# Performance work log

Hardware: AMD Instinct MI355X
Metric: run time of the kernel (lower is better)

The kernel has to match this reference:

```python
import jax, jax.numpy as jnp
import numpy as np

T, H, I, E, K = 4096, 2048, 1408, 8, 2  # tokens, hidden, intermediate, experts, top_k


def setup_inputs() -> dict:
    key = jax.random.key(0)
    ks = jax.random.split(key, 6)
    hidden_states = jax.random.normal(ks[0], (T, H), dtype=jnp.float32)
    gate_weight = jax.random.normal(ks[1], (E, H), dtype=jnp.float32) * 0.02  # fp32 gate, per source assert
    w13_weight = jax.random.randint(ks[2], (E, 2 * I, H), -127, 128, dtype=jnp.int8)
    w13_weight_scale = jax.random.uniform(ks[3], (E, 2 * I), dtype=jnp.float32, minval=0.5, maxval=1.5) * 0.005
    w2_weight = jax.random.randint(ks[4], (E, H, I), -127, 128, dtype=jnp.int8)
    w2_weight_scale = jax.random.uniform(ks[5], (E, H), dtype=jnp.float32, minval=0.5, maxval=1.5) * 0.005
    return dict(hidden_states=hidden_states, gate_weight=gate_weight,
                w13_weight=w13_weight, w13_weight_scale=w13_weight_scale,
                w2_weight=w2_weight, w2_weight_scale=w2_weight_scale)


def _dynamic_quant_i8(x):
    # per-token dynamic symmetric int8: scale = max|x|/127 (smooth scales default to ones)
    s = jnp.maximum(jnp.max(jnp.abs(x), axis=-1, keepdims=True) / 127.0, 1e-8)
    q = jnp.clip(jnp.round(x / s), -127.0, 127.0)
    return q, s


def reference(hidden_states, gate_weight, w13_weight, w13_weight_scale, w2_weight, w2_weight_scale):
    # --- gating: fp32 linear + topk softmax (renormalize=True) ---
    logits = hidden_states @ gate_weight.T              # [T, E]
    probs = jax.nn.softmax(logits, axis=-1)
    topv, topi = jax.lax.top_k(probs, K)                # [T, K]
    gates = topv / jnp.sum(topv, axis=-1, keepdims=True)
    # dense routing weights [T, E]: gate value where expert selected, else 0
    route = jnp.zeros((T, E), hidden_states.dtype).at[jnp.arange(T)[:, None], topi].add(gates)

    # --- dynamic per-token int8 quant of routed input (same token value for each of its K copies) ---
    q_in, s_in = _dynamic_quant_i8(hidden_states)       # [T, H], [T, 1]

    # --- grouped w8a8 GEMM (fc1) -> SwiGLU -> requant -> grouped GEMM (fc2) -> weighted combine ---
    def step(acc, xs):
        w13, s13, w2, s2w, r = xs                       # per-expert weights / route column [T]
        h1 = (q_in @ w13.T.astype(jnp.float32)) * s_in * s13[None, :]   # dequant fc1: [T, 2I]
        g, u = h1[:, :I], h1[:, I:]
        act = jax.nn.silu(g) * u                        # SwiGLU
        q_a, s_a = _dynamic_quant_i8(act)
        h2 = (q_a @ w2.T.astype(jnp.float32)) * s_a * s2w[None, :]      # dequant fc2: [T, H]
        return acc + r[:, None] * h2, None

    acc0 = jnp.zeros_like(hidden_states)
    out, _ = jax.lax.scan(step, acc0,
                          (w13_weight, w13_weight_scale, w2_weight, w2_weight_scale, route.T))
    return out
```

## Files before the change

### kernel.cpp

```cpp
#include <hip/hip_runtime.h>

#define T_TOK 4096
#define H_DIM 2048
#define I_DIM 1408
#define E_NUM 8
#define NI2   (2 * I_DIM)

typedef int v4i __attribute__((ext_vector_type(4)));

#define GLD_LDS16(gptr, lptr)                                                        \
  __builtin_amdgcn_global_load_lds(                                                  \
      (const __attribute__((address_space(1))) void*)(gptr),                         \
      (__attribute__((address_space(3))) void*)(lptr), 16, 0, 0)

__global__ __launch_bounds__(256) void pack_all(const int* __restrict__ w13,
                                                const int* __restrict__ w2,
                                                signed char* __restrict__ qw13,
                                                signed char* __restrict__ qw2,
                                                int n16a, int n16tot) {
  int i = blockIdx.x * 256 + threadIdx.x;
  if (i >= n16tot) return;
  const int* src;
  signed char* dst;
  int j;
  if (i < n16a) { src = w13; dst = qw13; j = i; }
  else          { src = w2;  dst = qw2;  j = i - n16a; }
  const int4* s4 = (const int4*)src + (size_t)j * 4;
  int4 v0 = s4[0], v1 = s4[1], v2 = s4[2], v3 = s4[3];
  union { signed char c[16]; int4 v; } pk;
  pk.c[0] = (signed char)v0.x;  pk.c[1] = (signed char)v0.y;
  pk.c[2] = (signed char)v0.z;  pk.c[3] = (signed char)v0.w;
  pk.c[4] = (signed char)v1.x;  pk.c[5] = (signed char)v1.y;
  pk.c[6] = (signed char)v1.z;  pk.c[7] = (signed char)v1.w;
  pk.c[8] = (signed char)v2.x;  pk.c[9] = (signed char)v2.y;
  pk.c[10] = (signed char)v2.z; pk.c[11] = (signed char)v2.w;
  pk.c[12] = (signed char)v3.x; pk.c[13] = (signed char)v3.y;
  pk.c[14] = (signed char)v3.z; pk.c[15] = (signed char)v3.w;
  ((int4*)dst)[j] = pk.v;
}

__global__ __launch_bounds__(256) void gate_route_quant(
    const float* __restrict__ hs, const float* __restrict__ gw,
    signed char* __restrict__ qin, float* __restrict__ s_in,
    int* __restrict__ tope, float* __restrict__ gts) {
  const int t = blockIdx.x;
  const int tid = threadIdx.x;
  const int lane = tid & 63;
  const int wave = tid >> 6;
  const float* row = hs + (size_t)t * H_DIM;

  const float4* r4 = (const float4*)row + tid * 2;
  float4 xa = r4[0], xb = r4[1];
  float x[8] = {xa.x, xa.y, xa.z, xa.w, xb.x, xb.y, xb.z, xb.w};

  double pd[8];
  for (int e = 0; e < 8; e++) pd[e] = 0.0;
  float am = 0.f;
  for (int j = 0; j < 8; j++) {
    float v = x[j];
    am = fmaxf(am, fabsf(v));
    int col = tid * 8 + j;
    for (int e = 0; e < 8; e++)
      pd[e] += (double)v * (double)gw[e * H_DIM + col];
  }
  for (int e = 0; e < 8; e++)
    for (int s = 32; s; s >>= 1) pd[e] += __shfl_down(pd[e], s);
  for (int s = 32; s; s >>= 1) am = fmaxf(am, __shfl_down(am, s));

  __shared__ double sred[4][8];
  __shared__ float sam[4];
  __shared__ float sbc;
  if (lane == 0) {
    for (int e = 0; e < 8; e++) sred[wave][e] = pd[e];
    sam[wave] = am;
  }
  __syncthreads();
  if (tid == 0) {
    float l[8];
    for (int e = 0; e < 8; e++)
      l[e] = (float)(sred[0][e] + sred[1][e] + sred[2][e] + sred[3][e]);
    float amx = fmaxf(fmaxf(sam[0], sam[1]), fmaxf(sam[2], sam[3]));
    float s = fmaxf(amx / 127.0f, 1e-8f);
    s_in[t] = s;
    sbc = s;
    int i1 = 0;
    for (int e = 1; e < 8; e++) if (l[e] > l[i1]) i1 = e;
    int i2 = -1;
    for (int e = 0; e < 8; e++) {
      if (e == i1) continue;
      if (i2 < 0 || l[e] > l[i2]) i2 = e;
    }
    float d = expf(l[i2] - l[i1]);
    tope[2 * t] = i1;     gts[2 * t] = 1.0f / (1.0f + d);
    tope[2 * t + 1] = i2; gts[2 * t + 1] = d / (1.0f + d);
  }
  __syncthreads();
  float s = sbc;
  union { signed char c[8]; unsigned long long u; } pk;
  for (int j = 0; j < 8; j++) {
    float q = rintf(x[j] / s);
    q = fminf(127.f, fmaxf(-127.f, q));
    pk.c[j] = (signed char)q;
  }
  ((unsigned long long*)(qin + (size_t)t * H_DIM))[tid] = pk.u;
}

__global__ __launch_bounds__(256) void build_lists(
    const int* __restrict__ tope, int* __restrict__ tok_list,
    int* __restrict__ epos, int* __restrict__ cnt) {
  const int e = blockIdx.x;
  const int tid = threadIdx.x;
  const int lane = tid & 63;
  const int wave = tid >> 6;
  __shared__ int wsum[4];
  __shared__ int base_s;
  if (tid == 0) base_s = 0;
  __syncthreads();
  for (int t0 = 0; t0 < T_TOK; t0 += 256) {
    int t = t0 + tid;
    int i1 = tope[2 * t], i2 = tope[2 * t + 1];
    int slot = (i1 == e) ? 0 : ((i2 == e) ? 1 : -1);
    unsigned long long m = __ballot(slot >= 0);
    int wpre = __popcll(m & ((1ull << lane) - 1ull));
    if (lane == 0) wsum[wave] = __popcll(m);
    __syncthreads();
    int pre = wpre;
    for (int w = 0; w < wave; w++) pre += wsum[w];
    int total = wsum[0] + wsum[1] + wsum[2] + wsum[3];
    int b = base_s;
    if (slot >= 0) {
      int pos = b + pre;
      tok_list[e * T_TOK + pos] = t;
      epos[2 * t + slot] = (e << 16) | pos;
    }
    __syncthreads();
    if (tid == 0) base_s = b + total;
  }
  __syncthreads();
  if (tid == 0) cnt[e] = base_s;
}

__global__ void calc_off(const int* __restrict__ cnt, int* __restrict__ off) {
  if (threadIdx.x == 0) {
    int s = 0;
    for (int e = 0; e < E_NUM; e++) { off[e] = s; s += cnt[e]; }
  }
}

__global__ __launch_bounds__(256, 3) void gemm1_silu(
    const signed char* __restrict__ qw13, const signed char* __restrict__ qin,
    const float* __restrict__ s_in, const float* __restrict__ s13,
    const int* __restrict__ tok_list, const int* __restrict__ cnt,
    const int* __restrict__ off, float* __restrict__ act,
    unsigned int* __restrict__ amax) {
  const int e = blockIdx.z;
  const int ce = cnt[e];
  const int m0 = blockIdx.y * 64;
  if (m0 >= ce) return;
  const int n0 = blockIdx.x * 128;

  __shared__ __align__(16) signed char As[64 * 64];
  __shared__ __align__(16) signed char Bg[128 * 64];
  __shared__ __align__(16) signed char Bu[128 * 64];

  const int tid = threadIdx.x;
  const int lane = tid & 63;
  const int wave = tid >> 6;
  const int quad = lane >> 4;
  const int ln = lane & 15;

  const int* tl = tok_list + e * T_TOK;
  const int rowA = tid >> 2;
  const int kc = (tid & 3) * 16;

  const int tA = tl[min(m0 + rowA, ce - 1)];
  const signed char* gA = qin + (size_t)tA * H_DIM + kc;
  const signed char* w13e = qw13 + (size_t)e * NI2 * H_DIM;
  const signed char* gBg0 = w13e + (size_t)(n0 + rowA) * H_DIM + kc;
  const signed char* gBg1 = w13e + (size_t)(n0 + rowA + 64) * H_DIM + kc;
  const signed char* gBu0 = gBg0 + (size_t)I_DIM * H_DIM;
  const signed char* gBu1 = gBg1 + (size_t)I_DIM * H_DIM;
  const int ldsA = tid * 16;
  const int lds1 = 4096 + ldsA;

  v4i accg[4][2], accu[4][2];
  v4i zero = {0, 0, 0, 0};
#pragma unroll
  for (int i = 0; i < 4; i++)
#pragma unroll
    for (int j = 0; j < 2; j++) { accg[i][j] = zero; accu[i][j] = zero; }

  for (int k0 = 0; k0 < H_DIM; k0 += 64) {
    __syncthreads();
    GLD_LDS16(gA + k0, As + ldsA);
    GLD_LDS16(gBg0 + k0, Bg + ldsA);
    GLD_LDS16(gBg1 + k0, Bg + lds1);
    GLD_LDS16(gBu0 + k0, Bu + ldsA);
    GLD_LDS16(gBu1 + k0, Bu + lds1);
    __syncthreads();

    v4i af[4], bgf[2], buf_[2];
#pragma unroll
    for (int mt = 0; mt < 4; mt++)
      af[mt] = *(const v4i*)(As + (mt * 16 + ln) * 64 + quad * 16);
#pragma unroll
    for (int nt = 0; nt < 2; nt++) {
      bgf[nt] = *(const v4i*)(Bg + (wave * 32 + nt * 16 + ln) * 64 + quad * 16);
      buf_[nt] = *(const v4i*)(Bu + (wave * 32 + nt * 16 + ln) * 64 + quad * 16);
    }
#pragma unroll
    for (int mt = 0; mt < 4; mt++)
#pragma unroll
      for (int nt = 0; nt < 2; nt++) {
        accg[mt][nt] = __builtin_amdgcn_mfma_i32_16x16x64_i8(af[mt], bgf[nt], accg[mt][nt], 0, 0, 0);
        accu[mt][nt] = __builtin_amdgcn_mfma_i32_16x16x64_i8(af[mt], buf_[nt], accu[mt][nt], 0, 0, 0);
      }
  }

  const float* s13e = s13 + e * NI2;
  float sg[2], su[2];
  int ncol[2];
#pragma unroll
  for (int nt = 0; nt < 2; nt++) {
    int n = n0 + wave * 32 + nt * 16 + ln;
    ncol[nt] = n;
    sg[nt] = s13e[n];
    su[nt] = s13e[I_DIM + n];
  }
  const int offe = off[e];
#pragma unroll
  for (int mt = 0; mt < 4; mt++) {
#pragma unroll
    for (int r = 0; r < 4; r++) {
      int mrel = m0 + mt * 16 + quad * 4 + r;
      bool valid = mrel < ce;
      int tok = tl[valid ? mrel : 0];
      float si = s_in[tok];
      int crow = offe + mrel;
      float* arow = act + (size_t)crow * I_DIM;
      float am = 0.f;
#pragma unroll
      for (int nt = 0; nt < 2; nt++) {
        float g = (float)accg[mt][nt][r] * si * sg[nt];
        float u = (float)accu[mt][nt][r] * si * su[nt];
        float a = g / (1.0f + expf(-g)) * u;
        if (valid) arow[ncol[nt]] = a;
        am = fmaxf(am, fabsf(a));
      }
      for (int s = 1; s < 16; s <<= 1) am = fmaxf(am, __shfl_xor(am, s, 16));
      if (valid && ln == 0) atomicMax(amax + crow, __float_as_uint(am));
    }
  }
}

__global__ __launch_bounds__(256) void quant_act(const float* __restrict__ act,
                                                 const unsigned int* __restrict__ amax,
                                                 signed char* __restrict__ qa,
                                                 float* __restrict__ s_a) {
  const int r = blockIdx.x;
  float am = __uint_as_float(amax[r]);
  float s = fmaxf(am / 127.0f, 1e-8f);
  if (threadIdx.x == 0) s_a[r] = s;
  const float* arow = act + (size_t)r * I_DIM;
  signed char* qrow = qa + (size_t)r * I_DIM;
  for (int j = threadIdx.x; j < I_DIM; j += 256) {
    float q = rintf(arow[j] / s);
    q = fminf(127.f, fmaxf(-127.f, q));
    qrow[j] = (signed char)q;
  }
}

__global__ __launch_bounds__(256, 4) void gemm2_h2(
    const signed char* __restrict__ qw2, const signed char* __restrict__ qa,
    const float* __restrict__ s_a, const float* __restrict__ s2w,
    const int* __restrict__ cnt, const int* __restrict__ off,
    float* __restrict__ h2s) {
  const int e = blockIdx.z;
  const int ce = cnt[e];
  const int m0 = blockIdx.y * 64;
  if (m0 >= ce) return;
  const int n0 = blockIdx.x * 128;
  const int offe = off[e];

  __shared__ __align__(16) signed char As[64 * 64];
  __shared__ __align__(16) signed char Bs[128 * 64];

  const int tid = threadIdx.x;
  const int lane = tid & 63;
  const int wave = tid >> 6;
  const int quad = lane >> 4;
  const int ln = lane & 15;

  const int rowA = tid >> 2;
  const int kc = (tid & 3) * 16;

  const signed char* gA = qa + (size_t)(offe + min(m0 + rowA, ce - 1)) * I_DIM + kc;
  const signed char* w2e = qw2 + (size_t)e * H_DIM * I_DIM;
  const signed char* gB0 = w2e + (size_t)(n0 + rowA) * I_DIM + kc;
  const signed char* gB1 = w2e + (size_t)(n0 + rowA + 64) * I_DIM + kc;
  const int ldsA = tid * 16;
  const int lds1 = 4096 + ldsA;

  v4i acc[4][2];
  v4i zero = {0, 0, 0, 0};
#pragma unroll
  for (int i = 0; i < 4; i++)
#pragma unroll
    for (int j = 0; j < 2; j++) acc[i][j] = zero;

  for (int k0 = 0; k0 < I_DIM; k0 += 64) {
    __syncthreads();
    GLD_LDS16(gA + k0, As + ldsA);
    GLD_LDS16(gB0 + k0, Bs + ldsA);
    GLD_LDS16(gB1 + k0, Bs + lds1);
    __syncthreads();

    v4i af[4], bf[2];
#pragma unroll
    for (int mt = 0; mt < 4; mt++)
      af[mt] = *(const v4i*)(As + (mt * 16 + ln) * 64 + quad * 16);
#pragma unroll
    for (int nt = 0; nt < 2; nt++)
      bf[nt] = *(const v4i*)(Bs + (wave * 32 + nt * 16 + ln) * 64 + quad * 16);
#pragma unroll
    for (int mt = 0; mt < 4; mt++)
#pragma unroll
      for (int nt = 0; nt < 2; nt++)
        acc[mt][nt] = __builtin_amdgcn_mfma_i32_16x16x64_i8(af[mt], bf[nt], acc[mt][nt], 0, 0, 0);
  }

  const float* s2e = s2w + e * H_DIM;
  float sw[2];
  int ncol[2];
#pragma unroll
  for (int nt = 0; nt < 2; nt++) {
    int n = n0 + wave * 32 + nt * 16 + ln;
    ncol[nt] = n;
    sw[nt] = s2e[n];
  }
#pragma unroll
  for (int mt = 0; mt < 4; mt++) {
#pragma unroll
    for (int r = 0; r < 4; r++) {
      int mrel = m0 + mt * 16 + quad * 4 + r;
      if (mrel >= ce) continue;
      float sa = s_a[offe + mrel];
      float* orow = h2s + (size_t)(offe + mrel) * H_DIM;
#pragma unroll
      for (int nt = 0; nt < 2; nt++)
        orow[ncol[nt]] = (float)acc[mt][nt][r] * sa * sw[nt];
    }
  }
}

__global__ __launch_bounds__(256) void gather_out(
    const float* __restrict__ h2s, const int* __restrict__ epos,
    const float* __restrict__ gts, const int* __restrict__ off,
    float* __restrict__ out) {
  const int t = blockIdx.x;
  int a = epos[2 * t], b = epos[2 * t + 1];
  float g1 = gts[2 * t], g2 = gts[2 * t + 1];
  int r1 = off[a >> 16] + (a & 0xffff);
  int r2 = off[b >> 16] + (b & 0xffff);
  const float4* R1 = (const float4*)(h2s + (size_t)r1 * H_DIM);
  const float4* R2 = (const float4*)(h2s + (size_t)r2 * H_DIM);
  float4* O = (float4*)(out + (size_t)t * H_DIM);
  for (int c = threadIdx.x; c < H_DIM / 4; c += 256) {
    float4 x = R1[c], y = R2[c];
    float4 z;
    z.x = g1 * x.x + g2 * y.x;
    z.y = g1 * x.y + g2 * y.y;
    z.z = g1 * x.z + g2 * y.z;
    z.w = g1 * x.w + g2 * y.w;
    O[c] = z;
  }
}

extern "C" void kernel_launch(void* const* d_in, const int* in_sizes, int n_in,
                              void* d_out, int out_size, void* d_ws, size_t ws_size,
                              hipStream_t stream) {
  const float* hs = (const float*)d_in[0];
  const float* gw = (const float*)d_in[1];
  const int* w13 = (const int*)d_in[2];
  const float* s13 = (const float*)d_in[3];
  const int* w2 = (const int*)d_in[4];
  const float* s2w = (const float*)d_in[5];
  float* out = (float*)d_out;

  char* ws = (char*)d_ws;
  size_t o = 0;
  auto take = [&](size_t b) {
    char* p = ws + o;
    o += (b + 255) & ~(size_t)255;
    return p;
  };
  signed char* qw13 = (signed char*)take((size_t)E_NUM * NI2 * H_DIM);
  signed char* qin = (signed char*)take((size_t)T_TOK * H_DIM);
  float* act = (float*)take((size_t)T_TOK * 2 * I_DIM * 4);
  float* h2s = (float*)qw13;
  signed char* qw2 = (signed char*)take((size_t)E_NUM * H_DIM * I_DIM);
  signed char* qa = (signed char*)take((size_t)T_TOK * 2 * I_DIM);
  float* sin_ = (float*)take((size_t)T_TOK * 4);
  float* sa = (float*)take((size_t)T_TOK * 2 * 4);
  unsigned int* amax = (unsigned int*)take((size_t)T_TOK * 2 * 4);
  int* tokl = (int*)take((size_t)E_NUM * T_TOK * 4);
  int* tope = (int*)take((size_t)T_TOK * 2 * 4);
  int* epos = (int*)take((size_t)T_TOK * 2 * 4);
  float* gts = (float*)take((size_t)T_TOK * 2 * 4);
  int* cnt = (int*)take(E_NUM * 4);
  int* off = (int*)take(E_NUM * 4);

  hipMemsetAsync(amax, 0, (size_t)T_TOK * 2 * 4, stream);

  {
    int n16a = E_NUM * NI2 * H_DIM / 16;
    int n16b = E_NUM * H_DIM * I_DIM / 16;
    int n16tot = n16a + n16b;
    pack_all<<<(n16tot + 255) / 256, 256, 0, stream>>>(w13, w2, qw13, qw2, n16a, n16tot);
  }
  gate_route_quant<<<T_TOK, 256, 0, stream>>>(hs, gw, qin, sin_, tope, gts);
  build_lists<<<E_NUM, 256, 0, stream>>>(tope, tokl, epos, cnt);
  calc_off<<<1, 64, 0, stream>>>(cnt, off);
  {
    dim3 g(I_DIM / 128, T_TOK / 64, E_NUM);
    gemm1_silu<<<g, 256, 0, stream>>>(qw13, qin, sin_, s13, tokl, cnt, off, act, amax);
  }
  quant_act<<<T_TOK * 2, 256, 0, stream>>>(act, amax, qa, sa);
  {
    dim3 g(H_DIM / 128, T_TOK / 64, E_NUM);
    gemm2_h2<<<g, 256, 0, stream>>>(qw2, qa, sa, s2w, cnt, off, h2s);
  }
  gather_out<<<T_TOK, 256, 0, stream>>>(h2s, epos, gts, off, out);
}
```

Before: 584.1 us.

## Replace LDS staging with direct register loads and double-buffered MFMA loops

Both grouped GEMMs drop the shared-memory tiles and __syncthreads barriers. Each wave now loads its A and B MFMA fragments straight from global memory into registers, using a two-stage register double buffer so loads for the next k-chunk overlap the current MFMAs. The grid is also reordered so blockIdx.x walks the token (M) tiles, which may keep the same weight columns hot in cache across neighbouring blocks. In exchange, the A tile is no longer shared across the four waves, so each wave refetches it from global memory or cache, and register pressure rises.

```diff
diff --git a/kernel.cpp b/kernel.cpp
--- a/kernel.cpp
+++ b/kernel.cpp
@@ -7,11 +7,6 @@
 #define NI2   (2 * I_DIM)
 
 typedef int v4i __attribute__((ext_vector_type(4)));
-
-#define GLD_LDS16(gptr, lptr)                                                        \
-  __builtin_amdgcn_global_load_lds(                                                  \
-      (const __attribute__((address_space(1))) void*)(gptr),                         \
-      (__attribute__((address_space(3))) void*)(lptr), 16, 0, 0)
 
 __global__ __launch_bounds__(256) void pack_all(const int* __restrict__ w13,
                                                 const int* __restrict__ w2,
@@ -155,33 +150,30 @@
     unsigned int* __restrict__ amax) {
   const int e = blockIdx.z;
   const int ce = cnt[e];
-  const int m0 = blockIdx.y * 64;
+  const int m0 = blockIdx.x * 64;
   if (m0 >= ce) return;
-  const int n0 = blockIdx.x * 128;
-
-  __shared__ __align__(16) signed char As[64 * 64];
-  __shared__ __align__(16) signed char Bg[128 * 64];
-  __shared__ __align__(16) signed char Bu[128 * 64];
-
-  const int tid = threadIdx.x;
-  const int lane = tid & 63;
-  const int wave = tid >> 6;
+  const int wave = threadIdx.x >> 6;
+  const int lane = threadIdx.x & 63;
   const int quad = lane >> 4;
   const int ln = lane & 15;
+  const int n0 = blockIdx.y * 128 + wave * 32;
 
   const int* tl = tok_list + e * T_TOK;
-  const int rowA = tid >> 2;
-  const int kc = (tid & 3) * 16;
-
-  const int tA = tl[min(m0 + rowA, ce - 1)];
-  const signed char* gA = qin + (size_t)tA * H_DIM + kc;
   const signed char* w13e = qw13 + (size_t)e * NI2 * H_DIM;
-  const signed char* gBg0 = w13e + (size_t)(n0 + rowA) * H_DIM + kc;
-  const signed char* gBg1 = w13e + (size_t)(n0 + rowA + 64) * H_DIM + kc;
-  const signed char* gBu0 = gBg0 + (size_t)I_DIM * H_DIM;
-  const signed char* gBu1 = gBg1 + (size_t)I_DIM * H_DIM;
-  const int ldsA = tid * 16;
-  const int lds1 = 4096 + ldsA;
+
+  const signed char* ap[4];
+#pragma unroll
+  for (int mt = 0; mt < 4; mt++) {
+    int mrel = min(m0 + mt * 16 + ln, ce - 1);
+    ap[mt] = qin + (size_t)tl[mrel] * H_DIM + quad * 16;
+  }
+  const signed char* bgp[2];
+  const signed char* bup[2];
+#pragma unroll
+  for (int nt = 0; nt < 2; nt++) {
+    bgp[nt] = w13e + (size_t)(n0 + nt * 16 + ln) * H_DIM + quad * 16;
+    bup[nt] = bgp[nt] + (size_t)I_DIM * H_DIM;
+  }
 
   v4i accg[4][2], accu[4][2];
   v4i zero = {0, 0, 0, 0};
@@ -190,39 +182,45 @@
 #pragma unroll
     for (int j = 0; j < 2; j++) { accg[i][j] = zero; accu[i][j] = zero; }
 
-  for (int k0 = 0; k0 < H_DIM; k0 += 64) {
-    __syncthreads();
-    GLD_LDS16(gA + k0, As + ldsA);
-    GLD_LDS16(gBg0 + k0, Bg + ldsA);
-    GLD_LDS16(gBg1 + k0, Bg + lds1);
-    GLD_LDS16(gBu0 + k0, Bu + ldsA);
-    GLD_LDS16(gBu1 + k0, Bu + lds1);
-    __syncthreads();
-
-    v4i af[4], bgf[2], buf_[2];
-#pragma unroll
-    for (int mt = 0; mt < 4; mt++)
-      af[mt] = *(const v4i*)(As + (mt * 16 + ln) * 64 + quad * 16);
-#pragma unroll
-    for (int nt = 0; nt < 2; nt++) {
-      bgf[nt] = *(const v4i*)(Bg + (wave * 32 + nt * 16 + ln) * 64 + quad * 16);
-      buf_[nt] = *(const v4i*)(Bu + (wave * 32 + nt * 16 + ln) * 64 + quad * 16);
-    }
-#pragma unroll
-    for (int mt = 0; mt < 4; mt++)
-#pragma unroll
-      for (int nt = 0; nt < 2; nt++) {
-        accg[mt][nt] = __builtin_amdgcn_mfma_i32_16x16x64_i8(af[mt], bgf[nt], accg[mt][nt], 0, 0, 0);
-        accu[mt][nt] = __builtin_amdgcn_mfma_i32_16x16x64_i8(af[mt], buf_[nt], accu[mt][nt], 0, 0, 0);
-      }
-  }
+  v4i aA[4], gA[2], uA[2];
+  v4i aB[4], gB[2], uB[2];
+
+#define LOADSET(Ar, Gr, Ur, K)                                         \
+  {                                                                    \
+    _Pragma("unroll") for (int mt = 0; mt < 4; mt++)                   \
+        Ar[mt] = *(const v4i*)(ap[mt] + (K));                          \
+    _Pragma("unroll") for (int nt = 0; nt < 2; nt++) {                 \
+      Gr[nt] = *(const v4i*)(bgp[nt] + (K));                           \
+      Ur[nt] = *(const v4i*)(bup[nt] + (K));                           \
+    }                                                                  \
+  }
+#define MFMASET(Ar, Gr, Ur)                                            \
+  {                                                                    \
+    _Pragma("unroll") for (int mt = 0; mt < 4; mt++)                   \
+        _Pragma("unroll") for (int nt = 0; nt < 2; nt++) {             \
+      accg[mt][nt] = __builtin_amdgcn_mfma_i32_16x16x64_i8(            \
+          Ar[mt], Gr[nt], accg[mt][nt], 0, 0, 0);                      \
+      accu[mt][nt] = __builtin_amdgcn_mfma_i32_16x16x64_i8(            \
+          Ar[mt], Ur[nt], accu[mt][nt], 0, 0, 0);                      \
+    }                                                                  \
+  }
+
+  LOADSET(aA, gA, uA, 0)
+  for (int k0 = 0; k0 < H_DIM; k0 += 128) {
+    LOADSET(aB, gB, uB, k0 + 64)
+    MFMASET(aA, gA, uA)
+    if (k0 + 128 < H_DIM) LOADSET(aA, gA, uA, k0 + 128)
+    MFMASET(aB, gB, uB)
+  }
+#undef LOADSET
+#undef MFMASET
 
   const float* s13e = s13 + e * NI2;
   float sg[2], su[2];
   int ncol[2];
 #pragma unroll
   for (int nt = 0; nt < 2; nt++) {
-    int n = n0 + wave * 32 + nt * 16 + ln;
+    int n = n0 + nt * 16 + ln;
     ncol[nt] = n;
     sg[nt] = s13e[n];
     su[nt] = s13e[I_DIM + n];
@@ -277,29 +275,27 @@
     float* __restrict__ h2s) {
   const int e = blockIdx.z;
   const int ce = cnt[e];
-  const int m0 = blockIdx.y * 64;
+  const int m0 = blockIdx.x * 64;
   if (m0 >= ce) return;
-  const int n0 = blockIdx.x * 128;
   const int offe = off[e];
-
-  __shared__ __align__(16) signed char As[64 * 64];
-  __shared__ __align__(16) signed char Bs[128 * 64];
-
-  const int tid = threadIdx.x;
-  const int lane = tid & 63;
-  const int wave = tid >> 6;
+  const int wave = threadIdx.x >> 6;
+  const int lane = threadIdx.x & 63;
   const int quad = lane >> 4;
   const int ln = lane & 15;
-
-  const int rowA = tid >> 2;
-  const int kc = (tid & 3) * 16;
-
-  const signed char* gA = qa + (size_t)(offe + min(m0 + rowA, ce - 1)) * I_DIM + kc;
+  const int n0 = blockIdx.y * 128 + wave * 32;
+
   const signed char* w2e = qw2 + (size_t)e * H_DIM * I_DIM;
-  const signed char* gB0 = w2e + (size_t)(n0 + rowA) * I_DIM + kc;
-  const signed char* gB1 = w2e + (size_t)(n0 + rowA + 64) * I_DIM + kc;
-  const int ldsA = tid * 16;
-  const int lds1 = 4096 + ldsA;
+
+  const signed char* ap[4];
+#pragma unroll
+  for (int mt = 0; mt < 4; mt++) {
+    int mrel = min(m0 + mt * 16 + ln, ce - 1);
+    ap[mt] = qa + (size_t)(offe + mrel) * I_DIM + quad * 16;
+  }
+  const signed char* bp[2];
+#pragma unroll
+  for (int nt = 0; nt < 2; nt++)
+    bp[nt] = w2e + (size_t)(n0 + nt * 16 + ln) * I_DIM + quad * 16;
 
   v4i acc[4][2];
   v4i zero = {0, 0, 0, 0};
@@ -308,33 +304,39 @@
 #pragma unroll
     for (int j = 0; j < 2; j++) acc[i][j] = zero;
 
-  for (int k0 = 0; k0 < I_DIM; k0 += 64) {
-    __syncthreads();
-    GLD_LDS16(gA + k0, As + ldsA);
-    GLD_LDS16(gB0 + k0, Bs + ldsA);
-    GLD_LDS16(gB1 + k0, Bs + lds1);
-    __syncthreads();
-
-    v4i af[4], bf[2];
-#pragma unroll
-    for (int mt = 0; mt < 4; mt++)
-      af[mt] = *(const v4i*)(As + (mt * 16 + ln) * 64 + quad * 16);
-#pragma unroll
-    for (int nt = 0; nt < 2; nt++)
-      bf[nt] = *(const v4i*)(Bs + (wave * 32 + nt * 16 + ln) * 64 + quad * 16);
-#pragma unroll
-    for (int mt = 0; mt < 4; mt++)
-#pragma unroll
-      for (int nt = 0; nt < 2; nt++)
-        acc[mt][nt] = __builtin_amdgcn_mfma_i32_16x16x64_i8(af[mt], bf[nt], acc[mt][nt], 0, 0, 0);
-  }
+  v4i aA[4], bA[2], aB[4], bB[2];
+
+#define LOADSET2(Ar, Br, K)                                            \
+  {                                                                    \
+    _Pragma("unroll") for (int mt = 0; mt < 4; mt++)                   \
+        Ar[mt] = *(const v4i*)(ap[mt] + (K));                          \
+    _Pragma("unroll") for (int nt = 0; nt < 2; nt++)                   \
+        Br[nt] = *(const v4i*)(bp[nt] + (K));                          \
+  }
+#define MFMASET2(Ar, Br)                                               \
+  {                                                                    \
+    _Pragma("unroll") for (int mt = 0; mt < 4; mt++)                   \
+        _Pragma("unroll") for (int nt = 0; nt < 2; nt++)               \
+            acc[mt][nt] = __builtin_amdgcn_mfma_i32_16x16x64_i8(       \
+                Ar[mt], Br[nt], acc[mt][nt], 0, 0, 0);                 \
+  }
+
+  LOADSET2(aA, bA, 0)
+  for (int k0 = 0; k0 < I_DIM; k0 += 128) {
+    LOADSET2(aB, bB, k0 + 64)
+    MFMASET2(aA, bA)
+    if (k0 + 128 < I_DIM) LOADSET2(aA, bA, k0 + 128)
+    MFMASET2(aB, bB)
+  }
+#undef LOADSET2
+#undef MFMASET2
 
   const float* s2e = s2w + e * H_DIM;
   float sw[2];
   int ncol[2];
 #pragma unroll
   for (int nt = 0; nt < 2; nt++) {
-    int n = n0 + wave * 32 + nt * 16 + ln;
+    int n = n0 + nt * 16 + ln;
     ncol[nt] = n;
     sw[nt] = s2e[n];
   }
@@ -422,12 +424,12 @@
   build_lists<<<E_NUM, 256, 0, stream>>>(tope, tokl, epos, cnt);
   calc_off<<<1, 64, 0, stream>>>(cnt, off);
   {
-    dim3 g(I_DIM / 128, T_TOK / 64, E_NUM);
+    dim3 g(T_TOK / 64, I_DIM / 128, E_NUM);
     gemm1_silu<<<g, 256, 0, stream>>>(qw13, qin, sin_, s13, tokl, cnt, off, act, amax);
   }
   quant_act<<<T_TOK * 2, 256, 0, stream>>>(act, amax, qa, sa);
   {
-    dim3 g(H_DIM / 128, T_TOK / 64, E_NUM);
+    dim3 g(T_TOK / 64, H_DIM / 128, E_NUM);
     gemm2_h2<<<g, 256, 0, stream>>>(qw2, qa, sa, s2w, cnt, off, h2s);
   }
   gather_out<<<T_TOK, 256, 0, stream>>>(h2s, epos, gts, off, out);
```

Result: slower. 1.057 ms (+81.0%).

## Pre-tile weights and activations into contiguous 64-wide K-chunk blocks for GEMMs

Applied to the files above, without the earlier changes.

Weights are repacked into per-128-row, per-64-K-chunk contiguous 8KB tiles, and routed activations are gathered into padded 64-row tiles (tile_a1 and the rewritten quant_act). The GEMM tile loads then become fully contiguous streams instead of strided row reads. The intermediate SwiGLU activation is stored as bf16 instead of fp32 to halve its traffic. The block grid is reordered so the M-tile index is fastest. The cost is an extra gather pass, padded workspace, and bf16 rounding before requantization, which could change some int8 values.

```diff
diff --git a/kernel.cpp b/kernel.cpp
--- a/kernel.cpp
+++ b/kernel.cpp
@@ -1,10 +1,12 @@
 #include <hip/hip_runtime.h>
+#include <hip/hip_bf16.h>
 
 #define T_TOK 4096
 #define H_DIM 2048
 #define I_DIM 1408
 #define E_NUM 8
 #define NI2   (2 * I_DIM)
+#define NMB   136
 
 typedef int v4i __attribute__((ext_vector_type(4)));
 
@@ -13,30 +15,43 @@
       (const __attribute__((address_space(1))) void*)(gptr),                         \
       (__attribute__((address_space(3))) void*)(lptr), 16, 0, 0)
 
-__global__ __launch_bounds__(256) void pack_all(const int* __restrict__ w13,
-                                                const int* __restrict__ w2,
-                                                signed char* __restrict__ qw13,
-                                                signed char* __restrict__ qw2,
-                                                int n16a, int n16tot) {
-  int i = blockIdx.x * 256 + threadIdx.x;
-  if (i >= n16tot) return;
+__global__ __launch_bounds__(256) void pack_tiled(
+    const int* __restrict__ w13, const int* __restrict__ w2,
+    signed char* __restrict__ qw13t, signed char* __restrict__ qw2t) {
+  const int id = blockIdx.x;
   const int* src;
   signed char* dst;
-  int j;
-  if (i < n16a) { src = w13; dst = qw13; j = i; }
-  else          { src = w2;  dst = qw2;  j = i - n16a; }
-  const int4* s4 = (const int4*)src + (size_t)j * 4;
-  int4 v0 = s4[0], v1 = s4[1], v2 = s4[2], v3 = s4[3];
-  union { signed char c[16]; int4 v; } pk;
-  pk.c[0] = (signed char)v0.x;  pk.c[1] = (signed char)v0.y;
-  pk.c[2] = (signed char)v0.z;  pk.c[3] = (signed char)v0.w;
-  pk.c[4] = (signed char)v1.x;  pk.c[5] = (signed char)v1.y;
-  pk.c[6] = (signed char)v1.z;  pk.c[7] = (signed char)v1.w;
-  pk.c[8] = (signed char)v2.x;  pk.c[9] = (signed char)v2.y;
-  pk.c[10] = (signed char)v2.z; pk.c[11] = (signed char)v2.w;
-  pk.c[12] = (signed char)v3.x; pk.c[13] = (signed char)v3.y;
-  pk.c[14] = (signed char)v3.z; pk.c[15] = (signed char)v3.w;
-  ((int4*)dst)[j] = pk.v;
+  int R, Kd, nb, kc, e;
+  if (id < 8 * 22 * 32) {
+    e = id / (22 * 32);
+    int r = id % (22 * 32);
+    nb = r / 32; kc = r % 32;
+    src = w13; dst = qw13t + (size_t)id * 8192; R = NI2; Kd = H_DIM;
+  } else {
+    int j = id - 8 * 22 * 32;
+    e = j / (16 * 22);
+    int r = j % (16 * 22);
+    nb = r / 22; kc = r % 22;
+    src = w2; dst = qw2t + (size_t)j * 8192; R = H_DIM; Kd = I_DIM;
+  }
+  const int tid = threadIdx.x;
+  const int seg = tid & 3;
+#pragma unroll
+  for (int h = 0; h < 2; h++) {
+    int row = h * 64 + (tid >> 2);
+    const int4* s4 = (const int4*)(src + ((size_t)(e * R + nb * 128 + row) * Kd + kc * 64 + seg * 16));
+    int4 v0 = s4[0], v1 = s4[1], v2 = s4[2], v3 = s4[3];
+    union { signed char c[16]; int4 v; } pk;
+    pk.c[0] = (signed char)v0.x;  pk.c[1] = (signed char)v0.y;
+    pk.c[2] = (signed char)v0.z;  pk.c[3] = (signed char)v0.w;
+    pk.c[4] = (signed char)v1.x;  pk.c[5] = (signed char)v1.y;
+    pk.c[6] = (signed char)v1.z;  pk.c[7] = (signed char)v1.w;
+    pk.c[8] = (signed char)v2.x;  pk.c[9] = (signed char)v2.y;
+    pk.c[10] = (signed char)v2.z; pk.c[11] = (signed char)v2.w;
+    pk.c[12] = (signed char)v3.x; pk.c[13] = (signed char)v3.y;
+    pk.c[14] = (signed char)v3.z; pk.c[15] = (signed char)v3.w;
+    *(int4*)(dst + h * 4096 + tid * 16) = pk.v;
+  }
 }
 
 __global__ __launch_bounds__(256) void gate_route_quant(
@@ -140,28 +155,52 @@
   if (tid == 0) cnt[e] = base_s;
 }
 
-__global__ void calc_off(const int* __restrict__ cnt, int* __restrict__ off) {
+__global__ void calc_off(const int* __restrict__ cnt, int* __restrict__ poff) {
   if (threadIdx.x == 0) {
-    int s = 0;
-    for (int e = 0; e < E_NUM; e++) { off[e] = s; s += cnt[e]; }
-  }
+    int p = 0;
+    for (int e = 0; e < E_NUM; e++) {
+      poff[e] = p;
+      p += ((cnt[e] + 63) >> 6) << 6;
+    }
+  }
+}
+
+__global__ __launch_bounds__(256) void tile_a1(
+    const signed char* __restrict__ qin, const int* __restrict__ tok_list,
+    const int* __restrict__ cnt, const int* __restrict__ poff,
+    signed char* __restrict__ qx1) {
+  const int e = blockIdx.y;
+  const int ce = cnt[e];
+  const int m0 = blockIdx.x * 64;
+  if (m0 >= ce) return;
+  const int pmb = (poff[e] >> 6) + blockIdx.x;
+  const int tid = threadIdx.x;
+  const int row = tid >> 2, seg = tid & 3;
+  const int tok = tok_list[e * T_TOK + min(m0 + row, ce - 1)];
+  const signed char* src = qin + (size_t)tok * H_DIM + seg * 16;
+  signed char* dstb = qx1 + (size_t)pmb * (32 * 4096) + tid * 16;
+#pragma unroll
+  for (int kc = 0; kc < 32; kc++)
+    *(int4*)(dstb + kc * 4096) = *(const int4*)(src + kc * 64);
 }
 
 __global__ __launch_bounds__(256, 3) void gemm1_silu(
-    const signed char* __restrict__ qw13, const signed char* __restrict__ qin,
+    const signed char* __restrict__ qw13t, const signed char* __restrict__ qx1,
     const float* __restrict__ s_in, const float* __restrict__ s13,
     const int* __restrict__ tok_list, const int* __restrict__ cnt,
-    const int* __restrict__ off, float* __restrict__ act,
+    const int* __restrict__ poff, __hip_bfloat16* __restrict__ act,
     unsigned int* __restrict__ amax) {
   const int e = blockIdx.z;
   const int ce = cnt[e];
-  const int m0 = blockIdx.y * 64;
+  const int m0 = blockIdx.x * 64;
   if (m0 >= ce) return;
-  const int n0 = blockIdx.x * 128;
-
-  __shared__ __align__(16) signed char As[64 * 64];
-  __shared__ __align__(16) signed char Bg[128 * 64];
-  __shared__ __align__(16) signed char Bu[128 * 64];
+  const int nb = blockIdx.y;
+  const int n0 = nb * 128;
+  const int pmb = (poff[e] >> 6) + blockIdx.x;
+
+  __shared__ __align__(16) signed char As[4096];
+  __shared__ __align__(16) signed char Bg[8192];
+  __shared__ __align__(16) signed char Bu[8192];
 
   const int tid = threadIdx.x;
   const int lane = tid & 63;
@@ -169,19 +208,10 @@
   const int quad = lane >> 4;
   const int ln = lane & 15;
 
-  const int* tl = tok_list + e * T_TOK;
-  const int rowA = tid >> 2;
-  const int kc = (tid & 3) * 16;
-
-  const int tA = tl[min(m0 + rowA, ce - 1)];
-  const signed char* gA = qin + (size_t)tA * H_DIM + kc;
-  const signed char* w13e = qw13 + (size_t)e * NI2 * H_DIM;
-  const signed char* gBg0 = w13e + (size_t)(n0 + rowA) * H_DIM + kc;
-  const signed char* gBg1 = w13e + (size_t)(n0 + rowA + 64) * H_DIM + kc;
-  const signed char* gBu0 = gBg0 + (size_t)I_DIM * H_DIM;
-  const signed char* gBu1 = gBg1 + (size_t)I_DIM * H_DIM;
-  const int ldsA = tid * 16;
-  const int lds1 = 4096 + ldsA;
+  const signed char* Ab = qx1 + (size_t)pmb * (32 * 4096) + tid * 16;
+  const signed char* Bgb = qw13t + (size_t)(e * 22 + nb) * 32 * 8192 + tid * 16;
+  const signed char* Bub = qw13t + (size_t)(e * 22 + nb + 11) * 32 * 8192 + tid * 16;
+  const int ldsu = (tid & ~63) * 16;
 
   v4i accg[4][2], accu[4][2];
   v4i zero = {0, 0, 0, 0};
@@ -190,13 +220,13 @@
 #pragma unroll
     for (int j = 0; j < 2; j++) { accg[i][j] = zero; accu[i][j] = zero; }
 
-  for (int k0 = 0; k0 < H_DIM; k0 += 64) {
-    __syncthreads();
-    GLD_LDS16(gA + k0, As + ldsA);
-    GLD_LDS16(gBg0 + k0, Bg + ldsA);
-    GLD_LDS16(gBg1 + k0, Bg + lds1);
-    GLD_LDS16(gBu0 + k0, Bu + ldsA);
-    GLD_LDS16(gBu1 + k0, Bu + lds1);
+  for (int kc = 0; kc < 32; kc++) {
+    __syncthreads();
+    GLD_LDS16(Ab + (size_t)kc * 4096, As + ldsu);
+    GLD_LDS16(Bgb + (size_t)kc * 8192, Bg + ldsu);
+    GLD_LDS16(Bgb + (size_t)kc * 8192 + 4096, Bg + 4096 + ldsu);
+    GLD_LDS16(Bub + (size_t)kc * 8192, Bu + ldsu);
+    GLD_LDS16(Bub + (size_t)kc * 8192 + 4096, Bu + 4096 + ldsu);
     __syncthreads();
 
     v4i af[4], bgf[2], buf_[2];
@@ -227,7 +257,8 @@
     sg[nt] = s13e[n];
     su[nt] = s13e[I_DIM + n];
   }
-  const int offe = off[e];
+  const int* tl = tok_list + e * T_TOK;
+  const int pbase = poff[e];
 #pragma unroll
   for (int mt = 0; mt < 4; mt++) {
 #pragma unroll
@@ -236,54 +267,76 @@
       bool valid = mrel < ce;
       int tok = tl[valid ? mrel : 0];
       float si = s_in[tok];
-      int crow = offe + mrel;
-      float* arow = act + (size_t)crow * I_DIM;
+      size_t prow = (size_t)(pbase + mrel);
+      __hip_bfloat16* arow = act + prow * I_DIM;
       float am = 0.f;
 #pragma unroll
       for (int nt = 0; nt < 2; nt++) {
         float g = (float)accg[mt][nt][r] * si * sg[nt];
         float u = (float)accu[mt][nt][r] * si * su[nt];
         float a = g / (1.0f + expf(-g)) * u;
-        if (valid) arow[ncol[nt]] = a;
+        if (valid) arow[ncol[nt]] = __float2bfloat16(a);
         am = fmaxf(am, fabsf(a));
       }
       for (int s = 1; s < 16; s <<= 1) am = fmaxf(am, __shfl_xor(am, s, 16));
-      if (valid && ln == 0) atomicMax(amax + crow, __float_as_uint(am));
-    }
-  }
-}
-
-__global__ __launch_bounds__(256) void quant_act(const float* __restrict__ act,
-                                                 const unsigned int* __restrict__ amax,
-                                                 signed char* __restrict__ qa,
-                                                 float* __restrict__ s_a) {
-  const int r = blockIdx.x;
-  float am = __uint_as_float(amax[r]);
-  float s = fmaxf(am / 127.0f, 1e-8f);
-  if (threadIdx.x == 0) s_a[r] = s;
-  const float* arow = act + (size_t)r * I_DIM;
-  signed char* qrow = qa + (size_t)r * I_DIM;
-  for (int j = threadIdx.x; j < I_DIM; j += 256) {
-    float q = rintf(arow[j] / s);
-    q = fminf(127.f, fmaxf(-127.f, q));
-    qrow[j] = (signed char)q;
+      if (valid && ln == 0) atomicMax(amax + prow, __float_as_uint(am));
+    }
+  }
+}
+
+__global__ __launch_bounds__(256) void quant_act(
+    const __hip_bfloat16* __restrict__ act, const unsigned int* __restrict__ amax,
+    const int* __restrict__ cnt, const int* __restrict__ poff,
+    signed char* __restrict__ qx2, float* __restrict__ s_a) {
+  const int e = blockIdx.y;
+  const int ce = cnt[e];
+  const int m0 = blockIdx.x * 64;
+  if (m0 >= ce) return;
+  const int pmb = (poff[e] >> 6) + blockIdx.x;
+  const int tid = threadIdx.x;
+  const int row = tid >> 2, seg = tid & 3;
+  const int mrel = m0 + row;
+  const bool valid = mrel < ce;
+  const size_t prow = (size_t)poff[e] + mrel;
+  float s = fmaxf(__uint_as_float(amax[prow]) / 127.0f, 1e-8f);
+  if (valid && seg == 0) s_a[prow] = s;
+  const unsigned short* arow = (const unsigned short*)(act + prow * I_DIM) + seg * 16;
+  signed char* dstb = qx2 + (size_t)pmb * (22 * 4096) + tid * 16;
+  for (int kc = 0; kc < 22; kc++) {
+    union { int4 v[2]; unsigned short u[16]; } in;
+    union { signed char c[16]; int4 v; } pk;
+    if (valid) {
+      in.v[0] = *(const int4*)(arow + kc * 64);
+      in.v[1] = *(const int4*)(arow + kc * 64 + 8);
+#pragma unroll
+      for (int j = 0; j < 16; j++) {
+        float f = __uint_as_float((unsigned)in.u[j] << 16);
+        float q = rintf(f / s);
+        q = fminf(127.f, fmaxf(-127.f, q));
+        pk.c[j] = (signed char)q;
+      }
+    } else {
+      pk.v = int4{0, 0, 0, 0};
+    }
+    *(int4*)(dstb + kc * 4096) = pk.v;
   }
 }
 
 __global__ __launch_bounds__(256, 4) void gemm2_h2(
-    const signed char* __restrict__ qw2, const signed char* __restrict__ qa,
+    const signed char* __restrict__ qw2t, const signed char* __restrict__ qx2,
     const float* __restrict__ s_a, const float* __restrict__ s2w,
-    const int* __restrict__ cnt, const int* __restrict__ off,
+    const int* __restrict__ cnt, const int* __restrict__ poff,
     float* __restrict__ h2s) {
   const int e = blockIdx.z;
   const int ce = cnt[e];
-  const int m0 = blockIdx.y * 64;
+  const int m0 = blockIdx.x * 64;
   if (m0 >= ce) return;
-  const int n0 = blockIdx.x * 128;
-  const int offe = off[e];
-
-  __shared__ __align__(16) signed char As[64 * 64];
-  __shared__ __align__(16) signed char Bs[128 * 64];
+  const int nb = blockIdx.y;
+  const int n0 = nb * 128;
+  const int pmb = (poff[e] >> 6) + blockIdx.x;
+
+  __shared__ __align__(16) signed char As[4096];
+  __shared__ __align__(16) signed char Bs[8192];
 
   const int tid = threadIdx.x;
   const int lane = tid & 63;
@@ -291,15 +344,9 @@
   const int quad = lane >> 4;
   const int ln = lane & 15;
 
-  const int rowA = tid >> 2;
-  const int kc = (tid & 3) * 16;
-
-  const signed char* gA = qa + (size_t)(offe + min(m0 + rowA, ce - 1)) * I_DIM + kc;
-  const signed char* w2e = qw2 + (size_t)e * H_DIM * I_DIM;
-  const signed char* gB0 = w2e + (size_t)(n0 + rowA) * I_DIM + kc;
-  const signed char* gB1 = w2e + (size_t)(n0 + rowA + 64) * I_DIM + kc;
-  const int ldsA = tid * 16;
-  const int lds1 = 4096 + ldsA;
+  const signed char* Ab = qx2 + (size_t)pmb * (22 * 4096) + tid * 16;
+  const signed char* Bb = qw2t + (size_t)(e * 16 + nb) * 22 * 8192 + tid * 16;
+  const int ldsu = (tid & ~63) * 16;
 
   v4i acc[4][2];
   v4i zero = {0, 0, 0, 0};
@@ -308,11 +355,11 @@
 #pragma unroll
     for (int j = 0; j < 2; j++) acc[i][j] = zero;
 
-  for (int k0 = 0; k0 < I_DIM; k0 += 64) {
-    __syncthreads();
-    GLD_LDS16(gA + k0, As + ldsA);
-    GLD_LDS16(gB0 + k0, Bs + ldsA);
-    GLD_LDS16(gB1 + k0, Bs + lds1);
+  for (int kc = 0; kc < 22; kc++) {
+    __syncthreads();
+    GLD_LDS16(Ab + (size_t)kc * 4096, As + ldsu);
+    GLD_LDS16(Bb + (size_t)kc * 8192, Bs + ldsu);
+    GLD_LDS16(Bb + (size_t)kc * 8192 + 4096, Bs + 4096 + ldsu);
     __syncthreads();
 
     v4i af[4], bf[2];
@@ -338,14 +385,16 @@
     ncol[nt] = n;
     sw[nt] = s2e[n];
   }
+  const int pbase = poff[e];
 #pragma unroll
   for (int mt = 0; mt < 4; mt++) {
 #pragma unroll
     for (int r = 0; r < 4; r++) {
       int mrel = m0 + mt * 16 + quad * 4 + r;
       if (mrel >= ce) continue;
-      float sa = s_a[offe + mrel];
-      float* orow = h2s + (size_t)(offe + mrel) * H_DIM;
+      size_t prow = (size_t)(pbase + mrel);
+      float sa = s_a[prow];
+      float* orow = h2s + prow * H_DIM;
 #pragma unroll
       for (int nt = 0; nt < 2; nt++)
         orow[ncol[nt]] = (float)acc[mt][nt][r] * sa * sw[nt];
@@ -355,13 +404,13 @@
 
 __global__ __launch_bounds__(256) void gather_out(
     const float* __restrict__ h2s, const int* __restrict__ epos,
-    const float* __restrict__ gts, const int* __restrict__ off,
+    const float* __restrict__ gts, const int* __restrict__ poff,
     float* __restrict__ out) {
   const int t = blockIdx.x;
   int a = epos[2 * t], b = epos[2 * t + 1];
   float g1 = gts[2 * t], g2 = gts[2 * t + 1];
-  int r1 = off[a >> 16] + (a & 0xffff);
-  int r2 = off[b >> 16] + (b & 0xffff);
+  int r1 = poff[a >> 16] + (a & 0xffff);
+  int r2 = poff[b >> 16] + (b & 0xffff);
   const float4* R1 = (const float4*)(h2s + (size_t)r1 * H_DIM);
   const float4* R2 = (const float4*)(h2s + (size_t)r2 * H_DIM);
   float4* O = (float4*)(out + (size_t)t * H_DIM);
@@ -387,6 +436,8 @@
   const float* s2w = (const float*)d_in[5];
   float* out = (float*)d_out;
 
+  const int PR = NMB * 64;
+
   char* ws = (char*)d_ws;
   size_t o = 0;
   auto take = [&](size_t b) {
@@ -394,41 +445,44 @@
     o += (b + 255) & ~(size_t)255;
     return p;
   };
-  signed char* qw13 = (signed char*)take((size_t)E_NUM * NI2 * H_DIM);
+  signed char* qw13t = (signed char*)take((size_t)E_NUM * NI2 * H_DIM);
   signed char* qin = (signed char*)take((size_t)T_TOK * H_DIM);
-  float* act = (float*)take((size_t)T_TOK * 2 * I_DIM * 4);
-  float* h2s = (float*)qw13;
-  signed char* qw2 = (signed char*)take((size_t)E_NUM * H_DIM * I_DIM);
-  signed char* qa = (signed char*)take((size_t)T_TOK * 2 * I_DIM);
+  signed char* qx1 = (signed char*)take((size_t)PR * H_DIM);
+  float* h2s = (float*)qw13t;
+  __hip_bfloat16* act = (__hip_bfloat16*)take((size_t)PR * I_DIM * 2);
+  signed char* qw2t = (signed char*)take((size_t)E_NUM * H_DIM * I_DIM);
+  signed char* qx2 = (signed char*)take((size_t)PR * I_DIM);
   float* sin_ = (float*)take((size_t)T_TOK * 4);
-  float* sa = (float*)take((size_t)T_TOK * 2 * 4);
-  unsigned int* amax = (unsigned int*)take((size_t)T_TOK * 2 * 4);
+  float* sa = (float*)take((size_t)PR * 4);
+  unsigned int* amax = (unsigned int*)take((size_t)PR * 4);
   int* tokl = (int*)take((size_t)E_NUM * T_TOK * 4);
   int* tope = (int*)take((size_t)T_TOK * 2 * 4);
   int* epos = (int*)take((size_t)T_TOK * 2 * 4);
   float* gts = (float*)take((size_t)T_TOK * 2 * 4);
   int* cnt = (int*)take(E_NUM * 4);
-  int* off = (int*)take(E_NUM * 4);
-
-  hipMemsetAsync(amax, 0, (size_t)T_TOK * 2 * 4, stream);
-
-  {
-    int n16a = E_NUM * NI2 * H_DIM / 16;
-    int n16b = E_NUM * H_DIM * I_DIM / 16;
-    int n16tot = n16a + n16b;
-    pack_all<<<(n16tot + 255) / 256, 256, 0, stream>>>(w13, w2, qw13, qw2, n16a, n16tot);
-  }
+  int* poff = (int*)take(E_NUM * 4);
+
+  hipMemsetAsync(amax, 0, (size_t)PR * 4, stream);
+
+  pack_tiled<<<8 * 22 * 32 + 8 * 16 * 22, 256, 0, stream>>>(w13, w2, qw13t, qw2t);
   gate_route_quant<<<T_TOK, 256, 0, stream>>>(hs, gw, qin, sin_, tope, gts);
   build_lists<<<E_NUM, 256, 0, stream>>>(tope, tokl, epos, cnt);
-  calc_off<<<1, 64, 0, stream>>>(cnt, off);
+  calc_off<<<1, 64, 0, stream>>>(cnt, poff);
   {
-    dim3 g(I_DIM / 128, T_TOK / 64, E_NUM);
-    gemm1_silu<<<g, 256, 0, stream>>>(qw13, qin, sin_, s13, tokl, cnt, off, act, amax);
-  }
-  quant_act<<<T_TOK * 2, 256, 0, stream>>>(act, amax, qa, sa);
+    dim3 g(64, 8);
+    tile_a1<<<g, 256, 0, stream>>>(qin, tokl, cnt, poff, qx1);
+  }
   {
-    dim3 g(H_DIM / 128, T_TOK / 64, E_NUM);
-    gemm2_h2<<<g, 256, 0, stream>>>(qw2, qa, sa, s2w, cnt, off, h2s);
-  }
-  gather_out<<<T_TOK, 256, 0, stream>>>(h2s, epos, gts, off, out);
-}
+    dim3 g(64, 11, 8);
+    gemm1_silu<<<g, 256, 0, stream>>>(qw13t, qx1, sin_, s13, tokl, cnt, poff, act, amax);
+  }
+  {
+    dim3 g(64, 8);
+    quant_act<<<g, 256, 0, stream>>>(act, amax, cnt, poff, qx2, sa);
+  }
+  {
+    dim3 g(64, 16, 8);
+    gemm2_h2<<<g, 256, 0, stream>>>(qw2t, qx2, sa, s2w, cnt, poff, h2s);
+  }
+  gather_out<<<T_TOK, 256, 0, stream>>>(h2s, epos, gts, poff, out);
+}
```

Measured after the change: 672.4 us. 1.15x slower.
